# Kernel optimization log

Measured on AMD Instinct MI355X. Metric: run time of the kernel, lower is better.

The kernel has to match this reference:

```python
import jax, jax.numpy as jnp
import numpy as np

D = 64
HID = 128
T_SPAN = (0.0, 1.0)


def _potential(q, Vw1, Vb1, Vw2, Vb2, Vw3, Vb3):
    # V(q): d -> hidden -> hidden -> 1, SiLU activations; returns [B]
    h = jax.nn.silu(q @ Vw1.T + Vb1)
    h = jax.nn.silu(h @ Vw2.T + Vb2)
    return (h @ Vw3.T + Vb3)[..., 0]


def setup_inputs() -> dict:
    key = jax.random.key(0)
    ks = jax.random.split(key, 12)
    B = 4096
    z = jax.random.normal(ks[0], (B, D), dtype=jnp.float32)
    # SeparableHamiltonian params
    mass_L = jnp.eye(D, dtype=jnp.float32) * 0.1 + jax.random.normal(ks[1], (D, D), dtype=jnp.float32) * 0.01
    s1 = 1.0 / np.sqrt(D)
    s2 = 1.0 / np.sqrt(HID)
    Vw1 = jax.random.uniform(ks[2], (HID, D), jnp.float32, -s1, s1)
    Vb1 = jax.random.uniform(ks[3], (HID,), jnp.float32, -s1, s1)
    Vw2 = jax.random.uniform(ks[4], (HID, HID), jnp.float32, -s2, s2)
    Vb2 = jax.random.uniform(ks[5], (HID,), jnp.float32, -s2, s2)
    Vw3 = jax.random.uniform(ks[6], (1, HID), jnp.float32, -s2, s2)
    Vb3 = jax.random.uniform(ks[7], (1,), jnp.float32, -s2, s2)
    # q/p encoders: Linear(d, d)
    qW = jax.random.uniform(ks[8], (D, D), jnp.float32, -s1, s1)
    qb = jax.random.uniform(ks[9], (D,), jnp.float32, -s1, s1)
    pW = jax.random.uniform(ks[10], (D, D), jnp.float32, -s1, s1)
    pb = jax.random.uniform(ks[11], (D,), jnp.float32, -s1, s1)
    return {"z": z, "mass_L": mass_L, "Vw1": Vw1, "Vb1": Vb1, "Vw2": Vw2, "Vb2": Vb2,
            "Vw3": Vw3, "Vb3": Vb3, "qW": qW, "qb": qb, "pW": pW, "pb": pb,
            "num_steps": 64}


def reference(z, mass_L, Vw1, Vb1, Vw2, Vb2, Vw3, Vb3, qW, qb, pW, pb, num_steps):
    # encode z -> phase space (q, p)
    q0 = z @ qW.T + qb
    p0 = z @ pW.T + pb
    # positive-definite mass matrix and its inverse
    M = mass_L @ mass_L.T + 0.01 * jnp.eye(D, dtype=mass_L.dtype)
    M_inv = jnp.linalg.inv(M)
    dt = (T_SPAN[1] - T_SPAN[0]) / num_steps

    gradV = jax.grad(lambda q: _potential(q, Vw1, Vb1, Vw2, Vb2, Vw3, Vb3).sum())

    def leapfrog(carry, _):
        q, p = carry
        p_half = p - 0.5 * dt * gradV(q)
        q_new = q + dt * jnp.einsum('de,be->bd', M_inv, p_half)
        p_new = p_half - 0.5 * dt * gradV(q_new)
        return (q_new, p_new), (q_new, p_new)

    (_, _), (q_steps, p_steps) = jax.lax.scan(leapfrog, (q0, p0), None, length=num_steps)
    # [B, T+1, d] trajectories (prepend initial state)
    q_traj = jnp.concatenate([q0[:, None], jnp.swapaxes(q_steps, 0, 1)], axis=1)
    p_traj = jnp.concatenate([p0[:, None], jnp.swapaxes(p_steps, 0, 1)], axis=1)
    # return phase-space trajectory [B, T+1, 2d]
    return jnp.concatenate([q_traj, p_traj], axis=-1)
```

## Files before the change

kernel.cpp:

```cpp
#include <hip/hip_runtime.h>
#include <hip/hip_bf16.h>
#include <cstdint>
#include <cstddef>

#define HID 128
#define DIM 64
#define ROWS 16
#define TMAIN 512

typedef float f32x4 __attribute__((ext_vector_type(4)));
typedef short s16x8 __attribute__((ext_vector_type(8)));
typedef unsigned int u32x2 __attribute__((ext_vector_type(2)));

__device__ __forceinline__ unsigned short f2bf(float x){
    union { float f; unsigned int u; } v; v.f = x;
    unsigned int r = v.u + 0x7FFFu + ((v.u >> 16) & 1u);
    return (unsigned short)(r >> 16);
}
__device__ __forceinline__ float bf2f(unsigned short b){
    union { unsigned int u; float f; } v; v.u = ((unsigned int)b) << 16;
    return v.f;
}
__device__ __forceinline__ unsigned pk2(float a, float b){
    union { __hip_bfloat162 h; unsigned u; } cv;
    cv.h = __float22bfloat162_rn(make_float2(a, b));
    return cv.u;
}
__device__ __forceinline__ s16x8 mk8(unsigned a, unsigned b, unsigned c, unsigned d){
    union { s16x8 s; unsigned u[4]; } t; t.u[0]=a; t.u[1]=b; t.u[2]=c; t.u[3]=d; return t.s;
}
__device__ __forceinline__ s16x8 ldfrag_f32(const float* base){
    f32x4 a = *(const f32x4*)base;
    f32x4 b = *(const f32x4*)(base + 4);
    return mk8(pk2(a[0],a[1]), pk2(a[2],a[3]), pk2(b[0],b[1]), pk2(b[2],b[3]));
}
__device__ __forceinline__ void ldfrag_hl(const float* base, s16x8& hi, s16x8& lo){
    f32x4 a = *(const f32x4*)base;
    f32x4 b = *(const f32x4*)(base + 4);
    float x[8] = {a[0],a[1],a[2],a[3],b[0],b[1],b[2],b[3]};
    union { s16x8 s; unsigned short us[8]; } H, L;
    #pragma unroll
    for (int j = 0; j < 8; ++j){
        unsigned short h = f2bf(x[j]);
        H.us[j] = h;
        L.us[j] = f2bf(x[j] - bf2f(h));
    }
    hi = H.s; lo = L.s;
}
__device__ __forceinline__ s16x8 ld_tr(const float* p, int stride){
    unsigned u[4];
    #pragma unroll
    for (int j = 0; j < 4; ++j){
        float a = p[(2*j)*stride];
        float b = p[(2*j+1)*stride];
        u[j] = pk2(a, b);
    }
    return mk8(u[0], u[1], u[2], u[3]);
}
__device__ __forceinline__ f32x4 mfma16(s16x8 a, s16x8 b, f32x4 c){
    return __builtin_amdgcn_mfma_f32_16x16x32_bf16(a, b, c, 0, 0, 0);
}
__device__ __forceinline__ void wr_hl(char* buf, int off, f32x4 v){
    unsigned short h[4], l[4];
    #pragma unroll
    for (int r = 0; r < 4; ++r){
        h[r] = f2bf(v[r]);
        l[r] = f2bf(v[r] - bf2f(h[r]));
    }
    u32x2 H, L;
    H[0] = (unsigned)h[0] | ((unsigned)h[1] << 16);
    H[1] = (unsigned)h[2] | ((unsigned)h[3] << 16);
    L[0] = (unsigned)l[0] | ((unsigned)l[1] << 16);
    L[1] = (unsigned)l[2] | ((unsigned)l[3] << 16);
    *(u32x2*)(buf + off) = H;
    *(u32x2*)(buf + 8192 + off) = L;
}
__device__ __forceinline__ void barrier_lds(){
    asm volatile("s_waitcnt lgkmcnt(0)" ::: "memory");
    __builtin_amdgcn_s_barrier();
    asm volatile("" ::: "memory");
}

__global__ __launch_bounds__(TMAIN) void k_main(
    const float* __restrict__ z, const float* __restrict__ L,
    const float* __restrict__ W1, const float* __restrict__ b1,
    const float* __restrict__ W2, const float* __restrict__ b2,
    const float* __restrict__ w3, const float* __restrict__ qW,
    const float* __restrict__ qb, const float* __restrict__ pW,
    const float* __restrict__ pb, const int* __restrict__ nsp,
    float* __restrict__ out)
{
    __shared__ __align__(16) char shm[65536];
    char* const sQb_ = shm;
    char* const sPb_ = shm + 2048;
    char* const sA1_ = shm + 4096;
    char* const sG2_ = shm + 8192;
    char* const sG1_ = shm + 12288;
    char* const sD1_ = shm + 16384;
    char* const bufA = shm;
    char* const bufB = shm + 16384;
    char* const bufC = shm + 32768;
    unsigned short* const smh = (unsigned short*)(shm + 32768);
    unsigned short* const sml = (unsigned short*)(shm + 40960);
    unsigned short* const w1mt = (unsigned short*)(shm + 49152);
    float* const fscr = (float*)(shm + 49152);

    const int tid = threadIdx.x;
    const int w = tid >> 6, lane = tid & 63;
    const int l15 = lane & 15, l4 = lane >> 4;
    const int sw = (l15 & 7) << 4;
    const int swu = (l15 & 7) << 3;
    const int m0 = w * 16;
    const int wq = w & 3;
    const int mq = wq * 16;
    const bool isQ = (w >= 4);
    const int NS = *nsp;
    const float dtv = 1.0f / (float)NS;
    const int TS = (NS + 1) * 128;
    const int b0 = blockIdx.x * ROWS;

    const int rt = w & 3, ct0 = (w >> 2) * 2;

    {
        s16x8 Ah[2], Al[2];
        #pragma unroll
        for (int kt = 0; kt < 2; ++kt)
            ldfrag_hl(L + (size_t)(16*rt + l15)*DIM + kt*32 + 8*l4, Ah[kt], Al[kt]);
        #pragma unroll
        for (int ct = 0; ct < 2; ++ct){
            const int n = 16*(ct0+ct) + l15;
            f32x4 acc = {0.f,0.f,0.f,0.f};
            #pragma unroll
            for (int kt = 0; kt < 2; ++kt){
                s16x8 Bh, Bl;
                ldfrag_hl(L + (size_t)n*DIM + kt*32 + 8*l4, Bh, Bl);
                acc = mfma16(Ah[kt], Bh, acc);
                acc = mfma16(Ah[kt], Bl, acc);
                acc = mfma16(Al[kt], Bh, acc);
            }
            #pragma unroll
            for (int r = 0; r < 4; ++r)
                if (16*rt + 4*l4 + r == n) acc[r] += 0.01f;
            wr_hl(bufC, n*128 + ((32*rt + 8*l4) ^ sw), acc);
        }
    }
    barrier_lds();

    {
        const int r = tid >> 3, c8 = (tid & 7) * 8;
        const unsigned short* mh = (const unsigned short*)bufC;
        s16x8 mv = *(const s16x8*)&mh[r*64 + (c8 ^ ((r&7)<<3))];
        float s = 0.f;
        #pragma unroll
        for (int j = 0; j < 8; ++j) s += fabsf(bf2f((unsigned short)mv[j]));
        fscr[tid] = s;
    }
    barrier_lds();
    if (tid < 64){
        float s = 0.f;
        #pragma unroll
        for (int j = 0; j < 8; ++j) s += fscr[tid*8 + j];
        fscr[512 + tid] = s;
    }
    barrier_lds();

    s16x8 Mh[2], Ml[2];
    {
        float mrs = 0.f;
        for (int i = 0; i < 64; ++i) mrs = fmaxf(mrs, fscr[512 + i]);
        const float cN = 0.995f / mrs;
        const int r = tid >> 3, c8 = (tid & 7) * 8;
        union { s16x8 s; unsigned short us[8]; } Xh, Xl;
        #pragma unroll
        for (int j = 0; j < 8; ++j){ Xh.us[j] = 0; Xl.us[j] = 0; }
        const int d = r - c8;
        if (d >= 0 && d < 8){
            unsigned short h = f2bf(cN);
            Xh.us[d] = h;
            Xl.us[d] = f2bf(cN - bf2f(h));
        }
        const int idx = r*64 + (c8 ^ ((r&7)<<3));
        *(s16x8*)((unsigned short*)bufA + idx) = Xh.s;
        *(s16x8*)((unsigned short*)(bufA + 8192) + idx) = Xl.s;
        #pragma unroll
        for (int kt = 0; kt < 2; ++kt){
            const int ao = (16*rt + l15)*128 + ((kt*64 + 16*l4) ^ sw);
            Mh[kt] = *(const s16x8*)(bufC + ao);
            Ml[kt] = *(const s16x8*)(bufC + 8192 + ao);
        }
    }
    barrier_lds();

    {
        char* pX = bufA; char* pY = bufB; char* pS = bufC;
        for (int it = 0; it < 12; ++it){
            #pragma unroll
            for (int ct = 0; ct < 2; ++ct){
                const int n = 16*(ct0+ct) + l15;
                f32x4 acc = {0.f,0.f,0.f,0.f};
                #pragma unroll
                for (int kt = 0; kt < 2; ++kt){
                    const int bo = n*128 + ((kt*64 + 16*l4) ^ sw);
                    s16x8 bh = *(const s16x8*)(pX + bo);
                    s16x8 bl = *(const s16x8*)(pX + 8192 + bo);
                    acc = mfma16(Mh[kt], bh, acc);
                    acc = mfma16(Mh[kt], bl, acc);
                    acc = mfma16(Ml[kt], bh, acc);
                }
                wr_hl(pY, n*128 + ((32*rt + 8*l4) ^ sw), acc);
            }
            barrier_lds();
            #pragma unroll
            for (int ct = 0; ct < 2; ++ct){
                const int n = 16*(ct0+ct) + l15;
                f32x4 acc = {0.f,0.f,0.f,0.f};
                #pragma unroll
                for (int kt = 0; kt < 2; ++kt){
                    const int ao = (16*rt + l15)*128 + ((kt*64 + 16*l4) ^ sw);
                    s16x8 ah = *(const s16x8*)(pY + ao);
                    s16x8 al = *(const s16x8*)(pY + 8192 + ao);
                    const int bo = n*128 + ((kt*64 + 16*l4) ^ sw);
                    s16x8 bh = *(const s16x8*)(pX + bo);
                    s16x8 bl = *(const s16x8*)(pX + 8192 + bo);
                    acc = mfma16(ah, bh, acc);
                    acc = mfma16(ah, bl, acc);
                    acc = mfma16(al, bh, acc);
                }
                const int xo = n*128 + ((32*rt + 8*l4) ^ sw);
                u32x2 H = *(const u32x2*)(pX + xo);
                u32x2 Lo = *(const u32x2*)(pX + 8192 + xo);
                f32x4 nx;
                #pragma unroll
                for (int r = 0; r < 4; ++r){
                    unsigned hu = (r < 2) ? H[0] : H[1];
                    unsigned lu = (r < 2) ? Lo[0] : Lo[1];
                    unsigned short hh = (unsigned short)((r & 1) ? (hu >> 16) : (hu & 0xffff));
                    unsigned short ll = (unsigned short)((r & 1) ? (lu >> 16) : (lu & 0xffff));
                    float xv = bf2f(hh) + bf2f(ll);
                    nx[r] = 2.0f * xv - acc[r];
                }
                wr_hl(pS, xo, nx);
            }
            barrier_lds();
            char* t = pX; pX = pS; pS = pY; pY = t;
        }
    }

    for (int i = tid; i < 1024; i += TMAIN)
        *(f32x4*)(shm + 32768 + 16*i) = *(const f32x4*)(shm + 16*i);
    barrier_lds();

    {
        const int h0 = w * 16;
        #pragma unroll
        for (int d0 = 0; d0 < 64; d0 += 16){
            f32x4 acc = {0.f,0.f,0.f,0.f};
            #pragma unroll
            for (int kt = 0; kt < 2; ++kt){
                s16x8 fB = ldfrag_f32(W1 + (size_t)(h0+l15)*DIM + kt*32 + 8*l4);
                const int ui = (d0+l15)*DIM + ((kt*32 + 8*l4) ^ swu);
                s16x8 aH = *(const s16x8*)&smh[ui];
                s16x8 aL = *(const s16x8*)&sml[ui];
                acc = mfma16(aH, fB, acc);
                acc = mfma16(aL, fB, acc);
            }
            #pragma unroll
            for (int r = 0; r < 4; ++r)
                w1mt[(size_t)(d0 + 4*l4 + r)*HID + h0 + l15] = f2bf(acc[r]);
        }
    }
    barrier_lds();

    s16x8 fW1[2], fW2[4], fW2T[4], fP4[4];
    #pragma unroll
    for (int kt = 0; kt < 2; ++kt)
        fW1[kt] = ldfrag_f32(W1 + (size_t)(m0+l15)*DIM + kt*32 + 8*l4);
    #pragma unroll
    for (int kt = 0; kt < 4; ++kt){
        fW2[kt]  = ldfrag_f32(W2 + (size_t)(m0+l15)*HID + kt*32 + 8*l4);
        fW2T[kt] = ld_tr(W2 + (size_t)(kt*32 + 8*l4)*HID + m0 + l15, HID);
    }
    if (isQ){
        #pragma unroll
        for (int kt = 0; kt < 4; ++kt)
            fP4[kt] = *(const s16x8*)&w1mt[(mq+l15)*HID + kt*32 + 8*l4];
    } else {
        #pragma unroll
        for (int kt = 0; kt < 4; ++kt)
            fP4[kt] = ld_tr(W1 + (size_t)(kt*32 + 8*l4)*DIM + mq + l15, DIM);
    }

    const f32x4 bb1 = *(const f32x4*)&b1[m0 + 4*l4];
    const f32x4 bb2 = *(const f32x4*)&b2[m0 + 4*l4];
    const f32x4 bw3 = *(const f32x4*)&w3[m0 + 4*l4];

    f32x4 master;
    {
        const float* zr = z + (size_t)(b0 + l15) * DIM;
        s16x8 bz0 = ldfrag_f32(zr + 8*l4);
        s16x8 bz1 = ldfrag_f32(zr + 32 + 8*l4);
        const float* eW = isQ ? qW : pW;
        const float* eb = isQ ? qb : pb;
        const float* wr = eW + (size_t)(mq + l15) * DIM;
        s16x8 fE0 = ldfrag_f32(wr + 8*l4);
        s16x8 fE1 = ldfrag_f32(wr + 32 + 8*l4);
        f32x4 acc = {0.f,0.f,0.f,0.f};
        acc = mfma16(fE0, bz0, acc);
        acc = mfma16(fE1, bz1, acc);
        f32x4 be = *(const f32x4*)&eb[mq + 4*l4];
        master = acc + be;
        if (isQ){
            u32x2 pr; pr[0] = pk2(master[0],master[1]); pr[1] = pk2(master[2],master[3]);
            *(u32x2*)(sQb_ + l15*128 + ((32*wq + 8*l4) ^ sw)) = pr;
        }
        const int ofs = isQ ? (mq + 4*l4) : (64 + mq + 4*l4);
        *(f32x4*)(out + (size_t)(b0 + l15) * TS + ofs) = master;
    }
    barrier_lds();

    f32x4 vm = {0.f,0.f,0.f,0.f};
    f32x4 pend = {0.f,0.f,0.f,0.f};

    for (int t = 0; t <= NS; ++t){
        {
            if (t >= 1){
                if (isQ)
                    *(f32x4*)(out + (size_t)(b0+l15)*TS + (size_t)t*128 + mq + 4*l4) = pend;
                else if (t >= 2)
                    *(f32x4*)(out + (size_t)(b0+l15)*TS + (size_t)(t-1)*128 + 64 + mq + 4*l4) = pend;
            }
            s16x8 bq0 = *(const s16x8*)(sQb_ + l15*128 + ((16*l4) ^ sw));
            s16x8 bq1 = *(const s16x8*)(sQb_ + l15*128 + ((64 + 16*l4) ^ sw));
            f32x4 a0 = {0.f,0.f,0.f,0.f}, a1v = {0.f,0.f,0.f,0.f};
            a0 = mfma16(fW1[0], bq0, a0);
            a1v = mfma16(fW1[1], bq1, a1v);
            f32x4 si, dv;
            #pragma unroll
            for (int r = 0; r < 4; ++r){
                float h = a0[r] + a1v[r] + bb1[r];
                float sg = 1.0f / (1.0f + __expf(-h));
                float s = h * sg;
                si[r] = s;
                dv[r] = sg + s * (1.0f - sg);
            }
            u32x2 pr; pr[0] = pk2(si[0],si[1]); pr[1] = pk2(si[2],si[3]);
            *(u32x2*)(sA1_ + l15*256 + ((2*m0 + 8*l4) ^ sw)) = pr;
            *(f32x4*)(sD1_ + l15*512 + ((4*m0 + 16*l4) ^ sw)) = dv;
        }
        barrier_lds();
        {
            f32x4 a0 = {0.f,0.f,0.f,0.f}, a1v = {0.f,0.f,0.f,0.f};
            #pragma unroll
            for (int kt = 0; kt < 2; ++kt){
                s16x8 ba0 = *(const s16x8*)(sA1_ + l15*256 + ((64*(2*kt) + 16*l4) ^ sw));
                s16x8 ba1 = *(const s16x8*)(sA1_ + l15*256 + ((64*(2*kt+1) + 16*l4) ^ sw));
                a0 = mfma16(fW2[2*kt], ba0, a0);
                a1v = mfma16(fW2[2*kt+1], ba1, a1v);
            }
            f32x4 g2;
            #pragma unroll
            for (int r = 0; r < 4; ++r){
                float h = a0[r] + a1v[r] + bb2[r];
                float sg = 1.0f / (1.0f + __expf(-h));
                g2[r] = bw3[r] * (sg * (1.0f + h * (1.0f - sg)));
            }
            u32x2 pr; pr[0] = pk2(g2[0],g2[1]); pr[1] = pk2(g2[2],g2[3]);
            *(u32x2*)(sG2_ + l15*256 + ((2*m0 + 8*l4) ^ sw)) = pr;
        }
        barrier_lds();
        {
            f32x4 a0 = {0.f,0.f,0.f,0.f}, a1v = {0.f,0.f,0.f,0.f};
            #pragma unroll
            for (int kt = 0; kt < 2; ++kt){
                s16x8 bg0 = *(const s16x8*)(sG2_ + l15*256 + ((64*(2*kt) + 16*l4) ^ sw));
                s16x8 bg1 = *(const s16x8*)(sG2_ + l15*256 + ((64*(2*kt+1) + 16*l4) ^ sw));
                a0 = mfma16(fW2T[2*kt], bg0, a0);
                a1v = mfma16(fW2T[2*kt+1], bg1, a1v);
            }
            f32x4 dv = *(const f32x4*)(sD1_ + l15*512 + ((4*m0 + 16*l4) ^ sw));
            f32x4 g1;
            #pragma unroll
            for (int r = 0; r < 4; ++r) g1[r] = (a0[r] + a1v[r]) * dv[r];
            u32x2 pr; pr[0] = pk2(g1[0],g1[1]); pr[1] = pk2(g1[2],g1[3]);
            *(u32x2*)(sG1_ + l15*256 + ((2*m0 + 8*l4) ^ sw)) = pr;
        }
        barrier_lds();
        if (!isQ){
            f32x4 a0 = {0.f,0.f,0.f,0.f}, a1v = {0.f,0.f,0.f,0.f};
            #pragma unroll
            for (int kt = 0; kt < 2; ++kt){
                s16x8 bg0 = *(const s16x8*)(sG1_ + l15*256 + ((64*(2*kt) + 16*l4) ^ sw));
                s16x8 bg1 = *(const s16x8*)(sG1_ + l15*256 + ((64*(2*kt+1) + 16*l4) ^ sw));
                a0 = mfma16(fP4[2*kt], bg0, a0);
                a1v = mfma16(fP4[2*kt+1], bg1, a1v);
            }
            if (t == 0){
                #pragma unroll
                for (int r = 0; r < 4; ++r) master[r] -= 0.5f * dtv * (a0[r] + a1v[r]);
                u32x2 pr; pr[0] = pk2(master[0],master[1]); pr[1] = pk2(master[2],master[3]);
                *(u32x2*)(sPb_ + l15*128 + ((32*wq + 8*l4) ^ sw)) = pr;
            } else {
                #pragma unroll
                for (int r = 0; r < 4; ++r){
                    float g = a0[r] + a1v[r];
                    pend[r] = master[r] - 0.5f * dtv * g;
                    master[r] -= dtv * g;
                }
            }
        } else if (t >= 1){
            f32x4 a0 = {0.f,0.f,0.f,0.f}, a1v = {0.f,0.f,0.f,0.f};
            #pragma unroll
            for (int kt = 0; kt < 2; ++kt){
                s16x8 bg0 = *(const s16x8*)(sG1_ + l15*256 + ((64*(2*kt) + 16*l4) ^ sw));
                s16x8 bg1 = *(const s16x8*)(sG1_ + l15*256 + ((64*(2*kt+1) + 16*l4) ^ sw));
                a0 = mfma16(fP4[2*kt], bg0, a0);
                a1v = mfma16(fP4[2*kt+1], bg1, a1v);
            }
            #pragma unroll
            for (int r = 0; r < 4; ++r){
                vm[r] -= dtv * (a0[r] + a1v[r]);
                master[r] += dtv * vm[r];
            }
            u32x2 pr; pr[0] = pk2(master[0],master[1]); pr[1] = pk2(master[2],master[3]);
            *(u32x2*)(sQb_ + l15*128 + ((32*wq + 8*l4) ^ sw)) = pr;
            pend = master;
        }
        barrier_lds();
        if (t == 0){
            if (isQ){
                s16x8 fMhi[2], fMlo[2];
                #pragma unroll
                for (int kt = 0; kt < 2; ++kt){
                    const int ui = (mq+l15)*DIM + ((kt*32 + 8*l4) ^ swu);
                    fMhi[kt] = *(const s16x8*)&smh[ui];
                    fMlo[kt] = *(const s16x8*)&sml[ui];
                }
                s16x8 bp0 = *(const s16x8*)(sPb_ + l15*128 + ((16*l4) ^ sw));
                s16x8 bp1 = *(const s16x8*)(sPb_ + l15*128 + ((64 + 16*l4) ^ sw));
                f32x4 aH = {0.f,0.f,0.f,0.f}, aL = {0.f,0.f,0.f,0.f};
                aH = mfma16(fMhi[0], bp0, aH);
                aH = mfma16(fMhi[1], bp1, aH);
                aL = mfma16(fMlo[0], bp0, aL);
                aL = mfma16(fMlo[1], bp1, aL);
                #pragma unroll
                for (int r = 0; r < 4; ++r){
                    vm[r] = aH[r] + aL[r];
                    master[r] += dtv * vm[r];
                }
                u32x2 pr; pr[0] = pk2(master[0],master[1]); pr[1] = pk2(master[2],master[3]);
                *(u32x2*)(sQb_ + l15*128 + ((32*wq + 8*l4) ^ sw)) = pr;
                pend = master;
            }
            barrier_lds();
        }
    }
    if (!isQ)
        *(f32x4*)(out + (size_t)(b0+l15)*TS + (size_t)NS*128 + 64 + mq + 4*l4) = pend;
}

extern "C" void kernel_launch(void* const* d_in, const int* in_sizes, int n_in,
                              void* d_out, int out_size, void* d_ws, size_t ws_size,
                              hipStream_t stream)
{
    const float* z  = (const float*)d_in[0];
    const float* L  = (const float*)d_in[1];
    const float* W1 = (const float*)d_in[2];
    const float* b1 = (const float*)d_in[3];
    const float* W2 = (const float*)d_in[4];
    const float* b2 = (const float*)d_in[5];
    const float* w3 = (const float*)d_in[6];
    const float* qW = (const float*)d_in[8];
    const float* qb = (const float*)d_in[9];
    const float* pW = (const float*)d_in[10];
    const float* pb = (const float*)d_in[11];
    const int* nsp  = (const int*)d_in[12];
    float* out = (float*)d_out;
    (void)d_ws; (void)ws_size;
    const int B = in_sizes[0] / DIM;

    k_main<<<B/ROWS, TMAIN, 0, stream>>>(z, L, W1, b1, W2, b2, w3, qW, qb, pW, pb, nsp, out);
}
```

Baseline: 151.7 us.

## Run leapfrog main loop on four waves with two hidden tiles each

The time-stepping loop now runs on only the first four waves of the 512-thread block. Each of those waves handles two 16-wide hidden tiles and both the q and p update paths, where before all eight waves handled one tile each, split into q and p roles. This is meant to cut barrier participation and per-wave fixed overhead in the serial step loop, at the cost of doubling per-wave MFMA work and register pressure while half the waves idle. It also replaces the serial 64-element max reduction with a wave shuffle reduction and hoists the W1 fragment loads out of the d0 loop.

```diff
diff --git a/kernel.cpp b/kernel.cpp
--- a/kernel.cpp
+++ b/kernel.cpp
@@ -110,10 +110,8 @@
     const int l15 = lane & 15, l4 = lane >> 4;
     const int sw = (l15 & 7) << 4;
     const int swu = (l15 & 7) << 3;
-    const int m0 = w * 16;
-    const int wq = w & 3;
-    const int mq = wq * 16;
-    const bool isQ = (w >= 4);
+    const bool cw = (w < 4);
+    const int mq = (w & 3) * 16;
     const int NS = *nsp;
     const float dtv = 1.0f / (float)NS;
     const int TS = (NS + 1) * 128;
@@ -166,8 +164,10 @@
 
     s16x8 Mh[2], Ml[2];
     {
-        float mrs = 0.f;
-        for (int i = 0; i < 64; ++i) mrs = fmaxf(mrs, fscr[512 + i]);
+        float mrs = fscr[512 + lane];
+        #pragma unroll
+        for (int off = 1; off < 64; off <<= 1)
+            mrs = fmaxf(mrs, __shfl_xor(mrs, off));
         const float cN = 0.995f / mrs;
         const int r = tid >> 3, c8 = (tid & 7) * 8;
         union { s16x8 s; unsigned short us[8]; } Xh, Xl;
@@ -252,18 +252,17 @@
 
     {
         const int h0 = w * 16;
+        s16x8 fB0 = ldfrag_f32(W1 + (size_t)(h0+l15)*DIM + 8*l4);
+        s16x8 fB1 = ldfrag_f32(W1 + (size_t)(h0+l15)*DIM + 32 + 8*l4);
         #pragma unroll
         for (int d0 = 0; d0 < 64; d0 += 16){
             f32x4 acc = {0.f,0.f,0.f,0.f};
-            #pragma unroll
-            for (int kt = 0; kt < 2; ++kt){
-                s16x8 fB = ldfrag_f32(W1 + (size_t)(h0+l15)*DIM + kt*32 + 8*l4);
-                const int ui = (d0+l15)*DIM + ((kt*32 + 8*l4) ^ swu);
-                s16x8 aH = *(const s16x8*)&smh[ui];
-                s16x8 aL = *(const s16x8*)&sml[ui];
-                acc = mfma16(aH, fB, acc);
-                acc = mfma16(aL, fB, acc);
-            }
+            const int u0 = (d0+l15)*DIM + ((8*l4) ^ swu);
+            const int u1 = (d0+l15)*DIM + ((32 + 8*l4) ^ swu);
+            acc = mfma16(*(const s16x8*)&smh[u0], fB0, acc);
+            acc = mfma16(*(const s16x8*)&sml[u0], fB0, acc);
+            acc = mfma16(*(const s16x8*)&smh[u1], fB1, acc);
+            acc = mfma16(*(const s16x8*)&sml[u1], fB1, acc);
             #pragma unroll
             for (int r = 0; r < 4; ++r)
                 w1mt[(size_t)(d0 + 4*l4 + r)*HID + h0 + l15] = f2bf(acc[r]);
@@ -271,163 +270,162 @@
     }
     barrier_lds();
 
-    s16x8 fW1[2], fW2[4], fW2T[4], fP4[4];
-    #pragma unroll
-    for (int kt = 0; kt < 2; ++kt)
-        fW1[kt] = ldfrag_f32(W1 + (size_t)(m0+l15)*DIM + kt*32 + 8*l4);
-    #pragma unroll
-    for (int kt = 0; kt < 4; ++kt){
-        fW2[kt]  = ldfrag_f32(W2 + (size_t)(m0+l15)*HID + kt*32 + 8*l4);
-        fW2T[kt] = ld_tr(W2 + (size_t)(kt*32 + 8*l4)*HID + m0 + l15, HID);
-    }
-    if (isQ){
-        #pragma unroll
-        for (int kt = 0; kt < 4; ++kt)
-            fP4[kt] = *(const s16x8*)&w1mt[(mq+l15)*HID + kt*32 + 8*l4];
-    } else {
-        #pragma unroll
-        for (int kt = 0; kt < 4; ++kt)
-            fP4[kt] = ld_tr(W1 + (size_t)(kt*32 + 8*l4)*DIM + mq + l15, DIM);
-    }
-
-    const f32x4 bb1 = *(const f32x4*)&b1[m0 + 4*l4];
-    const f32x4 bb2 = *(const f32x4*)&b2[m0 + 4*l4];
-    const f32x4 bw3 = *(const f32x4*)&w3[m0 + 4*l4];
-
-    f32x4 master;
-    {
+    s16x8 fW1[2][2], fW2[2][4], fW2T[2][4], fP4p[4], fP4q[4];
+    f32x4 bb1[2], bb2[2], bw3[2];
+    f32x4 master_q = {0.f,0.f,0.f,0.f}, master_p = {0.f,0.f,0.f,0.f};
+    if (cw){
+        #pragma unroll
+        for (int tt = 0; tt < 2; ++tt){
+            const int m0 = 32*w + 16*tt;
+            #pragma unroll
+            for (int kt = 0; kt < 2; ++kt)
+                fW1[tt][kt] = ldfrag_f32(W1 + (size_t)(m0+l15)*DIM + kt*32 + 8*l4);
+            #pragma unroll
+            for (int kt = 0; kt < 4; ++kt){
+                fW2[tt][kt]  = ldfrag_f32(W2 + (size_t)(m0+l15)*HID + kt*32 + 8*l4);
+                fW2T[tt][kt] = ld_tr(W2 + (size_t)(kt*32 + 8*l4)*HID + m0 + l15, HID);
+            }
+            bb1[tt] = *(const f32x4*)&b1[m0 + 4*l4];
+            bb2[tt] = *(const f32x4*)&b2[m0 + 4*l4];
+            bw3[tt] = *(const f32x4*)&w3[m0 + 4*l4];
+        }
+        #pragma unroll
+        for (int kt = 0; kt < 4; ++kt){
+            fP4q[kt] = *(const s16x8*)&w1mt[(mq+l15)*HID + kt*32 + 8*l4];
+            fP4p[kt] = ld_tr(W1 + (size_t)(kt*32 + 8*l4)*DIM + mq + l15, DIM);
+        }
         const float* zr = z + (size_t)(b0 + l15) * DIM;
         s16x8 bz0 = ldfrag_f32(zr + 8*l4);
         s16x8 bz1 = ldfrag_f32(zr + 32 + 8*l4);
-        const float* eW = isQ ? qW : pW;
-        const float* eb = isQ ? qb : pb;
-        const float* wr = eW + (size_t)(mq + l15) * DIM;
-        s16x8 fE0 = ldfrag_f32(wr + 8*l4);
-        s16x8 fE1 = ldfrag_f32(wr + 32 + 8*l4);
-        f32x4 acc = {0.f,0.f,0.f,0.f};
-        acc = mfma16(fE0, bz0, acc);
-        acc = mfma16(fE1, bz1, acc);
-        f32x4 be = *(const f32x4*)&eb[mq + 4*l4];
-        master = acc + be;
-        if (isQ){
-            u32x2 pr; pr[0] = pk2(master[0],master[1]); pr[1] = pk2(master[2],master[3]);
-            *(u32x2*)(sQb_ + l15*128 + ((32*wq + 8*l4) ^ sw)) = pr;
-        }
-        const int ofs = isQ ? (mq + 4*l4) : (64 + mq + 4*l4);
-        *(f32x4*)(out + (size_t)(b0 + l15) * TS + ofs) = master;
+        s16x8 fq0 = ldfrag_f32(qW + (size_t)(mq+l15)*DIM + 8*l4);
+        s16x8 fq1 = ldfrag_f32(qW + (size_t)(mq+l15)*DIM + 32 + 8*l4);
+        s16x8 fp0 = ldfrag_f32(pW + (size_t)(mq+l15)*DIM + 8*l4);
+        s16x8 fp1 = ldfrag_f32(pW + (size_t)(mq+l15)*DIM + 32 + 8*l4);
+        f32x4 aq = {0.f,0.f,0.f,0.f}, ap = {0.f,0.f,0.f,0.f};
+        aq = mfma16(fq0, bz0, aq); aq = mfma16(fq1, bz1, aq);
+        ap = mfma16(fp0, bz0, ap); ap = mfma16(fp1, bz1, ap);
+        master_q = aq + *(const f32x4*)&qb[mq + 4*l4];
+        master_p = ap + *(const f32x4*)&pb[mq + 4*l4];
+        u32x2 pr; pr[0] = pk2(master_q[0],master_q[1]); pr[1] = pk2(master_q[2],master_q[3]);
+        *(u32x2*)(sQb_ + l15*128 + ((32*(w&3) + 8*l4) ^ sw)) = pr;
+        *(f32x4*)(out + (size_t)(b0 + l15) * TS + mq + 4*l4) = master_q;
+        *(f32x4*)(out + (size_t)(b0 + l15) * TS + 64 + mq + 4*l4) = master_p;
     }
     barrier_lds();
 
     f32x4 vm = {0.f,0.f,0.f,0.f};
-    f32x4 pend = {0.f,0.f,0.f,0.f};
+    f32x4 pend_q = {0.f,0.f,0.f,0.f}, pend_p = {0.f,0.f,0.f,0.f};
 
     for (int t = 0; t <= NS; ++t){
-        {
+        if (cw){
             if (t >= 1){
-                if (isQ)
-                    *(f32x4*)(out + (size_t)(b0+l15)*TS + (size_t)t*128 + mq + 4*l4) = pend;
-                else if (t >= 2)
-                    *(f32x4*)(out + (size_t)(b0+l15)*TS + (size_t)(t-1)*128 + 64 + mq + 4*l4) = pend;
+                *(f32x4*)(out + (size_t)(b0+l15)*TS + (size_t)t*128 + mq + 4*l4) = pend_q;
+                if (t >= 2)
+                    *(f32x4*)(out + (size_t)(b0+l15)*TS + (size_t)(t-1)*128 + 64 + mq + 4*l4) = pend_p;
             }
             s16x8 bq0 = *(const s16x8*)(sQb_ + l15*128 + ((16*l4) ^ sw));
             s16x8 bq1 = *(const s16x8*)(sQb_ + l15*128 + ((64 + 16*l4) ^ sw));
-            f32x4 a0 = {0.f,0.f,0.f,0.f}, a1v = {0.f,0.f,0.f,0.f};
-            a0 = mfma16(fW1[0], bq0, a0);
-            a1v = mfma16(fW1[1], bq1, a1v);
-            f32x4 si, dv;
-            #pragma unroll
-            for (int r = 0; r < 4; ++r){
-                float h = a0[r] + a1v[r] + bb1[r];
-                float sg = 1.0f / (1.0f + __expf(-h));
-                float s = h * sg;
-                si[r] = s;
-                dv[r] = sg + s * (1.0f - sg);
-            }
-            u32x2 pr; pr[0] = pk2(si[0],si[1]); pr[1] = pk2(si[2],si[3]);
-            *(u32x2*)(sA1_ + l15*256 + ((2*m0 + 8*l4) ^ sw)) = pr;
-            *(f32x4*)(sD1_ + l15*512 + ((4*m0 + 16*l4) ^ sw)) = dv;
+            #pragma unroll
+            for (int tt = 0; tt < 2; ++tt){
+                const int m0 = 32*w + 16*tt;
+                f32x4 a0 = {0.f,0.f,0.f,0.f}, a1v = {0.f,0.f,0.f,0.f};
+                a0 = mfma16(fW1[tt][0], bq0, a0);
+                a1v = mfma16(fW1[tt][1], bq1, a1v);
+                f32x4 si, dv;
+                #pragma unroll
+                for (int r = 0; r < 4; ++r){
+                    float h = a0[r] + a1v[r] + bb1[tt][r];
+                    float sg = 1.0f / (1.0f + __expf(-h));
+                    float s = h * sg;
+                    si[r] = s;
+                    dv[r] = sg + s * (1.0f - sg);
+                }
+                u32x2 pr; pr[0] = pk2(si[0],si[1]); pr[1] = pk2(si[2],si[3]);
+                *(u32x2*)(sA1_ + l15*256 + ((2*m0 + 8*l4) ^ sw)) = pr;
+                *(f32x4*)(sD1_ + l15*512 + ((4*m0 + 16*l4) ^ sw)) = dv;
+            }
         }
         barrier_lds();
-        {
-            f32x4 a0 = {0.f,0.f,0.f,0.f}, a1v = {0.f,0.f,0.f,0.f};
-            #pragma unroll
-            for (int kt = 0; kt < 2; ++kt){
-                s16x8 ba0 = *(const s16x8*)(sA1_ + l15*256 + ((64*(2*kt) + 16*l4) ^ sw));
-                s16x8 ba1 = *(const s16x8*)(sA1_ + l15*256 + ((64*(2*kt+1) + 16*l4) ^ sw));
-                a0 = mfma16(fW2[2*kt], ba0, a0);
-                a1v = mfma16(fW2[2*kt+1], ba1, a1v);
-            }
-            f32x4 g2;
-            #pragma unroll
-            for (int r = 0; r < 4; ++r){
-                float h = a0[r] + a1v[r] + bb2[r];
-                float sg = 1.0f / (1.0f + __expf(-h));
-                g2[r] = bw3[r] * (sg * (1.0f + h * (1.0f - sg)));
-            }
-            u32x2 pr; pr[0] = pk2(g2[0],g2[1]); pr[1] = pk2(g2[2],g2[3]);
-            *(u32x2*)(sG2_ + l15*256 + ((2*m0 + 8*l4) ^ sw)) = pr;
+        if (cw){
+            s16x8 ba[4];
+            #pragma unroll
+            for (int kt = 0; kt < 4; ++kt)
+                ba[kt] = *(const s16x8*)(sA1_ + l15*256 + ((64*kt + 16*l4) ^ sw));
+            #pragma unroll
+            for (int tt = 0; tt < 2; ++tt){
+                const int m0 = 32*w + 16*tt;
+                f32x4 a0 = {0.f,0.f,0.f,0.f}, a1v = {0.f,0.f,0.f,0.f};
+                a0 = mfma16(fW2[tt][0], ba[0], a0);
+                a1v = mfma16(fW2[tt][1], ba[1], a1v);
+                a0 = mfma16(fW2[tt][2], ba[2], a0);
+                a1v = mfma16(fW2[tt][3], ba[3], a1v);
+                f32x4 g2;
+                #pragma unroll
+                for (int r = 0; r < 4; ++r){
+                    float h = a0[r] + a1v[r] + bb2[tt][r];
+                    float sg = 1.0f / (1.0f + __expf(-h));
+                    g2[r] = bw3[tt][r] * (sg * (1.0f + h * (1.0f - sg)));
+                }
+                u32x2 pr; pr[0] = pk2(g2[0],g2[1]); pr[1] = pk2(g2[2],g2[3]);
+                *(u32x2*)(sG2_ + l15*256 + ((2*m0 + 8*l4) ^ sw)) = pr;
+            }
         }
         barrier_lds();
-        {
-            f32x4 a0 = {0.f,0.f,0.f,0.f}, a1v = {0.f,0.f,0.f,0.f};
-            #pragma unroll
-            for (int kt = 0; kt < 2; ++kt){
-                s16x8 bg0 = *(const s16x8*)(sG2_ + l15*256 + ((64*(2*kt) + 16*l4) ^ sw));
-                s16x8 bg1 = *(const s16x8*)(sG2_ + l15*256 + ((64*(2*kt+1) + 16*l4) ^ sw));
-                a0 = mfma16(fW2T[2*kt], bg0, a0);
-                a1v = mfma16(fW2T[2*kt+1], bg1, a1v);
-            }
-            f32x4 dv = *(const f32x4*)(sD1_ + l15*512 + ((4*m0 + 16*l4) ^ sw));
-            f32x4 g1;
-            #pragma unroll
-            for (int r = 0; r < 4; ++r) g1[r] = (a0[r] + a1v[r]) * dv[r];
-            u32x2 pr; pr[0] = pk2(g1[0],g1[1]); pr[1] = pk2(g1[2],g1[3]);
-            *(u32x2*)(sG1_ + l15*256 + ((2*m0 + 8*l4) ^ sw)) = pr;
+        if (cw){
+            s16x8 bg[4];
+            #pragma unroll
+            for (int kt = 0; kt < 4; ++kt)
+                bg[kt] = *(const s16x8*)(sG2_ + l15*256 + ((64*kt + 16*l4) ^ sw));
+            #pragma unroll
+            for (int tt = 0; tt < 2; ++tt){
+                const int m0 = 32*w + 16*tt;
+                f32x4 a0 = {0.f,0.f,0.f,0.f}, a1v = {0.f,0.f,0.f,0.f};
+                a0 = mfma16(fW2T[tt][0], bg[0], a0);
+                a1v = mfma16(fW2T[tt][1], bg[1], a1v);
+                a0 = mfma16(fW2T[tt][2], bg[2], a0);
+                a1v = mfma16(fW2T[tt][3], bg[3], a1v);
+                f32x4 dv = *(const f32x4*)(sD1_ + l15*512 + ((4*m0 + 16*l4) ^ sw));
+                f32x4 g1;
+                #pragma unroll
+                for (int r = 0; r < 4; ++r) g1[r] = (a0[r] + a1v[r]) * dv[r];
+                u32x2 pr; pr[0] = pk2(g1[0],g1[1]); pr[1] = pk2(g1[2],g1[3]);
+                *(u32x2*)(sG1_ + l15*256 + ((2*m0 + 8*l4) ^ sw)) = pr;
+            }
         }
         barrier_lds();
-        if (!isQ){
-            f32x4 a0 = {0.f,0.f,0.f,0.f}, a1v = {0.f,0.f,0.f,0.f};
-            #pragma unroll
-            for (int kt = 0; kt < 2; ++kt){
-                s16x8 bg0 = *(const s16x8*)(sG1_ + l15*256 + ((64*(2*kt) + 16*l4) ^ sw));
-                s16x8 bg1 = *(const s16x8*)(sG1_ + l15*256 + ((64*(2*kt+1) + 16*l4) ^ sw));
-                a0 = mfma16(fP4[2*kt], bg0, a0);
-                a1v = mfma16(fP4[2*kt+1], bg1, a1v);
-            }
+        if (cw){
+            s16x8 bg[4];
+            #pragma unroll
+            for (int kt = 0; kt < 4; ++kt)
+                bg[kt] = *(const s16x8*)(sG1_ + l15*256 + ((64*kt + 16*l4) ^ sw));
+            f32x4 gp0 = {0.f,0.f,0.f,0.f}, gp1 = {0.f,0.f,0.f,0.f};
+            f32x4 gq0 = {0.f,0.f,0.f,0.f}, gq1 = {0.f,0.f,0.f,0.f};
+            gp0 = mfma16(fP4p[0], bg[0], gp0); gp1 = mfma16(fP4p[1], bg[1], gp1);
+            gq0 = mfma16(fP4q[0], bg[0], gq0); gq1 = mfma16(fP4q[1], bg[1], gq1);
+            gp0 = mfma16(fP4p[2], bg[2], gp0); gp1 = mfma16(fP4p[3], bg[3], gp1);
+            gq0 = mfma16(fP4q[2], bg[2], gq0); gq1 = mfma16(fP4q[3], bg[3], gq1);
             if (t == 0){
                 #pragma unroll
-                for (int r = 0; r < 4; ++r) master[r] -= 0.5f * dtv * (a0[r] + a1v[r]);
-                u32x2 pr; pr[0] = pk2(master[0],master[1]); pr[1] = pk2(master[2],master[3]);
-                *(u32x2*)(sPb_ + l15*128 + ((32*wq + 8*l4) ^ sw)) = pr;
+                for (int r = 0; r < 4; ++r) master_p[r] -= 0.5f * dtv * (gp0[r] + gp1[r]);
+                u32x2 pr; pr[0] = pk2(master_p[0],master_p[1]); pr[1] = pk2(master_p[2],master_p[3]);
+                *(u32x2*)(sPb_ + l15*128 + ((32*(w&3) + 8*l4) ^ sw)) = pr;
             } else {
                 #pragma unroll
                 for (int r = 0; r < 4; ++r){
-                    float g = a0[r] + a1v[r];
-                    pend[r] = master[r] - 0.5f * dtv * g;
-                    master[r] -= dtv * g;
-                }
-            }
-        } else if (t >= 1){
-            f32x4 a0 = {0.f,0.f,0.f,0.f}, a1v = {0.f,0.f,0.f,0.f};
-            #pragma unroll
-            for (int kt = 0; kt < 2; ++kt){
-                s16x8 bg0 = *(const s16x8*)(sG1_ + l15*256 + ((64*(2*kt) + 16*l4) ^ sw));
-                s16x8 bg1 = *(const s16x8*)(sG1_ + l15*256 + ((64*(2*kt+1) + 16*l4) ^ sw));
-                a0 = mfma16(fP4[2*kt], bg0, a0);
-                a1v = mfma16(fP4[2*kt+1], bg1, a1v);
-            }
-            #pragma unroll
-            for (int r = 0; r < 4; ++r){
-                vm[r] -= dtv * (a0[r] + a1v[r]);
-                master[r] += dtv * vm[r];
-            }
-            u32x2 pr; pr[0] = pk2(master[0],master[1]); pr[1] = pk2(master[2],master[3]);
-            *(u32x2*)(sQb_ + l15*128 + ((32*wq + 8*l4) ^ sw)) = pr;
-            pend = master;
+                    float g = gp0[r] + gp1[r];
+                    pend_p[r] = master_p[r] - 0.5f * dtv * g;
+                    master_p[r] -= dtv * g;
+                    vm[r] -= dtv * (gq0[r] + gq1[r]);
+                    master_q[r] += dtv * vm[r];
+                }
+                u32x2 pr; pr[0] = pk2(master_q[0],master_q[1]); pr[1] = pk2(master_q[2],master_q[3]);
+                *(u32x2*)(sQb_ + l15*128 + ((32*(w&3) + 8*l4) ^ sw)) = pr;
+                pend_q = master_q;
+            }
         }
         barrier_lds();
         if (t == 0){
-            if (isQ){
+            if (cw){
                 s16x8 fMhi[2], fMlo[2];
                 #pragma unroll
                 for (int kt = 0; kt < 2; ++kt){
@@ -445,17 +443,17 @@
                 #pragma unroll
                 for (int r = 0; r < 4; ++r){
                     vm[r] = aH[r] + aL[r];
-                    master[r] += dtv * vm[r];
-                }
-                u32x2 pr; pr[0] = pk2(master[0],master[1]); pr[1] = pk2(master[2],master[3]);
-                *(u32x2*)(sQb_ + l15*128 + ((32*wq + 8*l4) ^ sw)) = pr;
-                pend = master;
+                    master_q[r] += dtv * vm[r];
+                }
+                u32x2 pr; pr[0] = pk2(master_q[0],master_q[1]); pr[1] = pk2(master_q[2],master_q[3]);
+                *(u32x2*)(sQb_ + l15*128 + ((32*(w&3) + 8*l4) ^ sw)) = pr;
+                pend_q = master_q;
             }
             barrier_lds();
         }
     }
-    if (!isQ)
-        *(f32x4*)(out + (size_t)(b0+l15)*TS + (size_t)NS*128 + 64 + mq + 4*l4) = pend;
+    if (cw)
+        *(f32x4*)(out + (size_t)(b0+l15)*TS + (size_t)NS*128 + 64 + mq + 4*l4) = pend_p;
 }
 
 extern "C" void kernel_launch(void* const* d_in, const int* in_sizes, int n_in,
```

Result: no change. 151.6 us (-0.0%).

## Split mass-inverse and weight-transpose precompute into a separate prep kernel

Applied to the files above, without the earlier changes.

Moves the per-block computation of the mass matrix, its Newton-Schulz inverse and the W1·M_inv product into a two-block prep kernel that writes bf16 results to workspace, which also stores pre-transposed bf16 W1 and W2. The main kernel then loads these fragments from global memory and no longer needs 64KB of LDS, so its shared memory shrinks. The goal is to stop every one of the 256 blocks from repeating the same setup and to raise occupancy. The cost is an extra launch that is serialized before the main kernel, plus global reads of the precomputed fragments.

```diff
diff --git a/kernel.cpp b/kernel.cpp
--- a/kernel.cpp
+++ b/kernel.cpp
@@ -47,16 +47,6 @@
     }
     hi = H.s; lo = L.s;
 }
-__device__ __forceinline__ s16x8 ld_tr(const float* p, int stride){
-    unsigned u[4];
-    #pragma unroll
-    for (int j = 0; j < 4; ++j){
-        float a = p[(2*j)*stride];
-        float b = p[(2*j+1)*stride];
-        u[j] = pk2(a, b);
-    }
-    return mk8(u[0], u[1], u[2], u[3]);
-}
 __device__ __forceinline__ f32x4 mfma16(s16x8 a, s16x8 b, f32x4 c){
     return __builtin_amdgcn_mfma_f32_16x16x32_bf16(a, b, c, 0, 0, 0);
 }
@@ -81,44 +71,39 @@
     asm volatile("" ::: "memory");
 }
 
-__global__ __launch_bounds__(TMAIN) void k_main(
-    const float* __restrict__ z, const float* __restrict__ L,
-    const float* __restrict__ W1, const float* __restrict__ b1,
-    const float* __restrict__ W2, const float* __restrict__ b2,
-    const float* __restrict__ w3, const float* __restrict__ qW,
-    const float* __restrict__ qb, const float* __restrict__ pW,
-    const float* __restrict__ pb, const int* __restrict__ nsp,
-    float* __restrict__ out)
+#define WS_W1MT 0
+#define WS_MHI  16384
+#define WS_MLO  24576
+#define WS_W1T  32768
+#define WS_W2T  49152
+
+__global__ __launch_bounds__(512) void k_prep(
+    const float* __restrict__ L, const float* __restrict__ W1,
+    const float* __restrict__ W2, char* __restrict__ ws)
 {
-    __shared__ __align__(16) char shm[65536];
-    char* const sQb_ = shm;
-    char* const sPb_ = shm + 2048;
-    char* const sA1_ = shm + 4096;
-    char* const sG2_ = shm + 8192;
-    char* const sG1_ = shm + 12288;
-    char* const sD1_ = shm + 16384;
-    char* const bufA = shm;
-    char* const bufB = shm + 16384;
-    char* const bufC = shm + 32768;
-    unsigned short* const smh = (unsigned short*)(shm + 32768);
-    unsigned short* const sml = (unsigned short*)(shm + 40960);
-    unsigned short* const w1mt = (unsigned short*)(shm + 49152);
-    float* const fscr = (float*)(shm + 49152);
-
     const int tid = threadIdx.x;
+    if (blockIdx.x == 1){
+        unsigned short* w1t = (unsigned short*)(ws + WS_W1T);
+        unsigned short* w2t = (unsigned short*)(ws + WS_W2T);
+        for (int i = tid; i < HID*DIM; i += 512){
+            int h = i >> 6, d = i & 63;
+            w1t[d*HID + h] = f2bf(W1[i]);
+        }
+        for (int i = tid; i < HID*HID; i += 512){
+            int c2 = i >> 7, c1 = i & 127;
+            w2t[c1*HID + c2] = f2bf(W2[i]);
+        }
+        return;
+    }
+    __shared__ __align__(16) char nbuf[51712];
+    char* const bufA = nbuf;
+    char* const bufB = nbuf + 16384;
+    char* const bufC = nbuf + 32768;
+    float* const fscr = (float*)(nbuf + 49152);
+
     const int w = tid >> 6, lane = tid & 63;
     const int l15 = lane & 15, l4 = lane >> 4;
     const int sw = (l15 & 7) << 4;
-    const int swu = (l15 & 7) << 3;
-    const int m0 = w * 16;
-    const int wq = w & 3;
-    const int mq = wq * 16;
-    const bool isQ = (w >= 4);
-    const int NS = *nsp;
-    const float dtv = 1.0f / (float)NS;
-    const int TS = (NS + 1) * 128;
-    const int b0 = blockIdx.x * ROWS;
-
     const int rt = w & 3, ct0 = (w >> 2) * 2;
 
     {
@@ -166,8 +151,10 @@
 
     s16x8 Mh[2], Ml[2];
     {
-        float mrs = 0.f;
-        for (int i = 0; i < 64; ++i) mrs = fmaxf(mrs, fscr[512 + i]);
+        float mrs = fscr[512 + lane];
+        #pragma unroll
+        for (int off = 1; off < 64; off <<= 1)
+            mrs = fmaxf(mrs, __shfl_xor(mrs, off));
         const float cN = 0.995f / mrs;
         const int r = tid >> 3, c8 = (tid & 7) * 8;
         union { s16x8 s; unsigned short us[8]; } Xh, Xl;
@@ -246,30 +233,73 @@
         }
     }
 
-    for (int i = tid; i < 1024; i += TMAIN)
-        *(f32x4*)(shm + 32768 + 16*i) = *(const f32x4*)(shm + 16*i);
-    barrier_lds();
+    {
+        unsigned short* mhi = (unsigned short*)(ws + WS_MHI);
+        unsigned short* mlo = (unsigned short*)(ws + WS_MLO);
+        const unsigned short* xh = (const unsigned short*)bufA;
+        const unsigned short* xl = (const unsigned short*)(bufA + 8192);
+        for (int i = tid; i < 4096; i += 512){
+            int r = i >> 6, c = i & 63;
+            int si = r*64 + (c ^ ((r&7)<<3));
+            mhi[i] = xh[si];
+            mlo[i] = xl[si];
+        }
+    }
 
     {
         const int h0 = w * 16;
+        s16x8 fB0 = ldfrag_f32(W1 + (size_t)(h0+l15)*DIM + 8*l4);
+        s16x8 fB1 = ldfrag_f32(W1 + (size_t)(h0+l15)*DIM + 32 + 8*l4);
+        const unsigned short* xh = (const unsigned short*)bufA;
+        const unsigned short* xl = (const unsigned short*)(bufA + 8192);
+        unsigned short* w1mt = (unsigned short*)(ws + WS_W1MT);
         #pragma unroll
         for (int d0 = 0; d0 < 64; d0 += 16){
             f32x4 acc = {0.f,0.f,0.f,0.f};
-            #pragma unroll
-            for (int kt = 0; kt < 2; ++kt){
-                s16x8 fB = ldfrag_f32(W1 + (size_t)(h0+l15)*DIM + kt*32 + 8*l4);
-                const int ui = (d0+l15)*DIM + ((kt*32 + 8*l4) ^ swu);
-                s16x8 aH = *(const s16x8*)&smh[ui];
-                s16x8 aL = *(const s16x8*)&sml[ui];
-                acc = mfma16(aH, fB, acc);
-                acc = mfma16(aL, fB, acc);
-            }
+            const int u0 = (d0+l15)*64 + ((8*l4) ^ ((l15&7)<<3));
+            const int u1 = (d0+l15)*64 + ((32 + 8*l4) ^ ((l15&7)<<3));
+            acc = mfma16(*(const s16x8*)&xh[u0], fB0, acc);
+            acc = mfma16(*(const s16x8*)&xl[u0], fB0, acc);
+            acc = mfma16(*(const s16x8*)&xh[u1], fB1, acc);
+            acc = mfma16(*(const s16x8*)&xl[u1], fB1, acc);
             #pragma unroll
             for (int r = 0; r < 4; ++r)
                 w1mt[(size_t)(d0 + 4*l4 + r)*HID + h0 + l15] = f2bf(acc[r]);
         }
     }
-    barrier_lds();
+}
+
+__global__ __launch_bounds__(TMAIN) void k_main(
+    const float* __restrict__ z, const float* __restrict__ W1,
+    const float* __restrict__ b1, const float* __restrict__ W2,
+    const float* __restrict__ b2, const float* __restrict__ w3,
+    const float* __restrict__ qW, const float* __restrict__ qb,
+    const float* __restrict__ pW, const float* __restrict__ pb,
+    const int* __restrict__ nsp, const char* __restrict__ ws,
+    float* __restrict__ out)
+{
+    __shared__ __align__(16) char sQb_[ROWS*128], sPb_[ROWS*128];
+    __shared__ __align__(16) char sA1_[ROWS*256], sG2_[ROWS*256], sG1_[ROWS*256];
+    __shared__ __align__(16) char sD1_[ROWS*512];
+
+    const int tid = threadIdx.x;
+    const int w = tid >> 6, lane = tid & 63;
+    const int l15 = lane & 15, l4 = lane >> 4;
+    const int sw = (l15 & 7) << 4;
+    const int m0 = w * 16;
+    const int wq = w & 3;
+    const int mq = wq * 16;
+    const bool isQ = (w >= 4);
+    const int NS = *nsp;
+    const float dtv = 1.0f / (float)NS;
+    const int TS = (NS + 1) * 128;
+    const int b0 = blockIdx.x * ROWS;
+
+    const unsigned short* wsW1MT = (const unsigned short*)(ws + WS_W1MT);
+    const unsigned short* wsW1T  = (const unsigned short*)(ws + WS_W1T);
+    const unsigned short* wsW2T  = (const unsigned short*)(ws + WS_W2T);
+    const unsigned short* wsMhi  = (const unsigned short*)(ws + WS_MHI);
+    const unsigned short* wsMlo  = (const unsigned short*)(ws + WS_MLO);
 
     s16x8 fW1[2], fW2[4], fW2T[4], fP4[4];
     #pragma unroll
@@ -278,16 +308,13 @@
     #pragma unroll
     for (int kt = 0; kt < 4; ++kt){
         fW2[kt]  = ldfrag_f32(W2 + (size_t)(m0+l15)*HID + kt*32 + 8*l4);
-        fW2T[kt] = ld_tr(W2 + (size_t)(kt*32 + 8*l4)*HID + m0 + l15, HID);
-    }
-    if (isQ){
+        fW2T[kt] = *(const s16x8*)&wsW2T[(m0+l15)*HID + kt*32 + 8*l4];
+    }
+    {
+        const unsigned short* wp4 = isQ ? wsW1MT : wsW1T;
         #pragma unroll
         for (int kt = 0; kt < 4; ++kt)
-            fP4[kt] = *(const s16x8*)&w1mt[(mq+l15)*HID + kt*32 + 8*l4];
-    } else {
-        #pragma unroll
-        for (int kt = 0; kt < 4; ++kt)
-            fP4[kt] = ld_tr(W1 + (size_t)(kt*32 + 8*l4)*DIM + mq + l15, DIM);
+            fP4[kt] = *(const s16x8*)&wp4[(mq+l15)*HID + kt*32 + 8*l4];
     }
 
     const f32x4 bb1 = *(const f32x4*)&b1[m0 + 4*l4];
@@ -431,9 +458,8 @@
                 s16x8 fMhi[2], fMlo[2];
                 #pragma unroll
                 for (int kt = 0; kt < 2; ++kt){
-                    const int ui = (mq+l15)*DIM + ((kt*32 + 8*l4) ^ swu);
-                    fMhi[kt] = *(const s16x8*)&smh[ui];
-                    fMlo[kt] = *(const s16x8*)&sml[ui];
+                    fMhi[kt] = *(const s16x8*)&wsMhi[(mq+l15)*DIM + kt*32 + 8*l4];
+                    fMlo[kt] = *(const s16x8*)&wsMlo[(mq+l15)*DIM + kt*32 + 8*l4];
                 }
                 s16x8 bp0 = *(const s16x8*)(sPb_ + l15*128 + ((16*l4) ^ sw));
                 s16x8 bp1 = *(const s16x8*)(sPb_ + l15*128 + ((64 + 16*l4) ^ sw));
@@ -475,8 +501,9 @@
     const float* pb = (const float*)d_in[11];
     const int* nsp  = (const int*)d_in[12];
     float* out = (float*)d_out;
-    (void)d_ws; (void)ws_size;
+    char* ws = (char*)d_ws;
     const int B = in_sizes[0] / DIM;
 
-    k_main<<<B/ROWS, TMAIN, 0, stream>>>(z, L, W1, b1, W2, b2, w3, qW, qb, pW, pb, nsp, out);
-}
+    k_prep<<<2, 512, 0, stream>>>(L, W1, W2, ws);
+    k_main<<<B/ROWS, TMAIN, 0, stream>>>(z, W1, b1, W2, b2, w3, qW, qb, pW, pb, nsp, ws, out);
+}
```

After: 129.7 us. 1.17x faster.
